# Kernel tuning notes

Measured on AMD Instinct MI355X. Metric: run time of the kernel, lower is better.

The kernel has to match this reference:

```python
import jax, jax.numpy as jnp
import numpy as np
from jax import lax

STRIDE = (1, 1)
PADDING = ((1, 1), (1, 1))


@jax.custom_vjp
def ternary_quantize(w):
    """Quantize OIHW weights to {-1,0,+1} with per-output-channel scale alpha."""
    abs_w = jnp.abs(w)
    delta = 0.7 * abs_w.mean(axis=(1, 2, 3), keepdims=True)          # [O,1,1,1]
    ternary = jnp.where(w > delta, 1.0, jnp.where(w < -delta, -1.0, 0.0)).astype(w.dtype)
    mask = ternary != 0
    count = jnp.maximum(mask.sum(axis=(1, 2, 3), keepdims=True), 1).astype(w.dtype)
    alpha = (abs_w * mask.astype(w.dtype)).sum(axis=(1, 2, 3), keepdims=True) / count
    return ternary, alpha


def _tq_fwd(w):
    return ternary_quantize(w), w


def _tq_bwd(w, grads):
    g_ternary, _g_alpha = grads  # STE: grad_alpha is discarded
    g = jnp.where(jnp.abs(w) > 1.0, 0.0, g_ternary)
    return (g,)


ternary_quantize.defvjp(_tq_fwd, _tq_bwd)


def setup_inputs() -> dict:
    key = jax.random.key(0)
    kx, kw = jax.random.split(key)
    x = jax.random.normal(kx, (32, 256, 56, 56), dtype=jnp.float32)
    # kaiming_normal fan_out: std = sqrt(2 / (out_ch * kH * kW))
    std = np.sqrt(2.0 / (256 * 3 * 3)).astype(np.float32)
    weight = jax.random.normal(kw, (256, 256, 3, 3), dtype=jnp.float32) * std
    return {"x": x, "weight": weight}


def reference(x, weight):
    ternary, alpha = ternary_quantize(weight)
    scaled_w = alpha * ternary  # values in {-alpha_o, 0, +alpha_o}
    return lax.conv_general_dilated(
        x, scaled_w,
        window_strides=STRIDE,
        padding=PADDING,
        dimension_numbers=("NCHW", "OIHW", "NCHW"),
    )
```

## Files before the change

### kernel.cpp

```cpp
#include <hip/hip_runtime.h>
#include <hip/hip_bf16.h>

typedef unsigned short u16;
typedef __bf16 bf16x8 __attribute__((ext_vector_type(8)));
typedef float f32x4 __attribute__((ext_vector_type(4)));
typedef u16 u16x8 __attribute__((ext_vector_type(8)));

__device__ __forceinline__ u16 f2bf(float f) {
    __bf16 h = (__bf16)f;
    return __builtin_bit_cast(unsigned short, h);
}

__device__ __forceinline__ void gl_lds16(const u16* g, u16* l) {
    __builtin_amdgcn_global_load_lds(
        (const __attribute__((address_space(1))) void*)g,
        (__attribute__((address_space(3))) void*)l, 16, 0, 0);
}

__global__ __launch_bounds__(256) void prep_kernel(
        const float* __restrict__ x, const float* __restrict__ w,
        u16* __restrict__ xp, u16* __restrict__ wp,
        float* __restrict__ alpha) {
    __shared__ double red[4];
    __shared__ double red2[4];
    __shared__ int    redc[4];

    int bid = blockIdx.x;
    int t = threadIdx.x;

    if (bid < 256) {
        int o = bid;
        const float* wo = w + (size_t)o * 2304;
        float v[9];
        double asum = 0.0;
        #pragma unroll
        for (int i = 0; i < 9; ++i) { v[i] = wo[t * 9 + i]; asum += fabs((double)v[i]); }
        #pragma unroll
        for (int off = 32; off > 0; off >>= 1) asum += __shfl_down(asum, off, 64);
        int wv = t >> 6, lane = t & 63;
        if (lane == 0) red[wv] = asum;
        __syncthreads();
        double delta = 0.7 * ((red[0] + red[1] + red[2] + red[3]) / 2304.0);

        int mt = o >> 7, ol = o & 127;
        int ks = (t >> 3) & 7, c = t & 7;
        double msum = 0.0; int cnt = 0;
        #pragma unroll
        for (int i = 0; i < 9; ++i) {
            double f = (double)v[i];
            float tv = 0.f;
            if (f > delta) tv = 1.f;
            else if (f < -delta) tv = -1.f;
            if (tv != 0.f) { msum += fabs(f); cnt++; }
            int kc = i * 4 + (t >> 6);
            wp[((((size_t)mt * 36 + kc) * 8 + ks) * 128 + ol) * 8 + c] = f2bf(tv);
        }
        #pragma unroll
        for (int off = 32; off > 0; off >>= 1) {
            msum += __shfl_down(msum, off, 64);
            cnt  += __shfl_down(cnt,  off, 64);
        }
        if (lane == 0) { red2[wv] = msum; redc[wv] = cnt; }
        __syncthreads();
        if (t == 0) {
            double ms = red2[0] + red2[1] + red2[2] + red2[3];
            int cn = redc[0] + redc[1] + redc[2] + redc[3];
            alpha[o] = (float)(ms / (double)(cn > 0 ? cn : 1));
        }
        return;
    }

    int pbid = bid - 256;
    int img  = pbid & 31;
    int cihi = (pbid >> 5) & 31;
    int z    = pbid >> 10;

    if (z == 12 && t >= 64) {
        int bt = t - 64;
        if (bt < 228) {
            int hp, wl;
            if (bt < 58)       { hp = 0;            wl = bt; }
            else if (bt < 116) { hp = 57;           wl = bt - 58; }
            else if (bt < 172) { hp = bt - 116 + 1; wl = 0; }
            else               { hp = bt - 172 + 1; wl = 57; }
            u16x8 zv = {};
            *(u16x8*)(xp + (((size_t)(img * 32 + cihi) * 58 + hp) * 58 + wl) * 8) = zv;
        }
        return;
    }

    int c = z * 256 + t;
    int h = c / 56, wq = c - h * 56;
    const float* xb = x + ((size_t)(img * 256 + cihi * 8)) * 3136 + c;
    u16x8 ov;
    #pragma unroll
    for (int j = 0; j < 8; ++j) ov[j] = f2bf(xb[(size_t)j * 3136]);
    *(u16x8*)(xp + (((size_t)(img * 32 + cihi) * 58 + (h + 1)) * 58 + (wq + 1)) * 8) = ov;
}

#define STAGE_CHUNK(KC, LA, LB) do {                                        \
    int f_ = (KC) >> 2;                                                      \
    int kh_ = f_ / 3, kw_ = f_ - kh_ * 3;                                    \
    int ci8_ = ((KC) & 3) * 8;                                               \
    unsigned bhw_ = (unsigned)kh_ * 464u + (unsigned)kw_ * 8u;               \
    unsigned bo0_ = (unsigned)(ci8_ + s0) * 26912u + bhw_;                   \
    unsigned bo1_ = (unsigned)(ci8_ + s1) * 26912u + bhw_;                   \
    const u16* aC_ = aTile + (size_t)(KC) * 8192;                            \
    _Pragma("unroll")                                                        \
    for (int q_ = 0; q_ < 4; ++q_) {                                         \
        int seg_ = wave * 4 + q_;                                            \
        gl_lds16(aC_ + seg_ * 512 + lane * 8, (LA) + seg_ * 512);            \
    }                                                                        \
    gl_lds16(bB0 + bo0_, (LB) + s0 * 1024);                                  \
    gl_lds16(bB1 + bo0_, (LB) + s0 * 1024 + 512);                            \
    gl_lds16(bB0 + bo1_, (LB) + s1 * 1024);                                  \
    gl_lds16(bB1 + bo1_, (LB) + s1 * 1024 + 512);                            \
} while (0)

#define HALF_ITER(LA, LB, VMSTR, STAGE_KC, DO_STAGE) do {                    \
    asm volatile("s_waitcnt " VMSTR ::: "memory");                           \
    __builtin_amdgcn_sched_barrier(0);                                       \
    __builtin_amdgcn_s_barrier();                                            \
    __builtin_amdgcn_sched_barrier(0);                                       \
    bf16x8 af_[2][4], bf_[2][4];                                             \
    _Pragma("unroll")                                                        \
    for (int kk_ = 0; kk_ < 2; ++kk_) {                                      \
        int ks_ = kk_ * 4 + quad;                                            \
        _Pragma("unroll")                                                    \
        for (int i_ = 0; i_ < 4; ++i_)                                       \
            af_[kk_][i_] = *(const bf16x8*)&(LA)[(ks_ * 128 + wm + i_ * 16 + row16) * 8]; \
        _Pragma("unroll")                                                    \
        for (int j_ = 0; j_ < 4; ++j_)                                       \
            bf_[kk_][j_] = *(const bf16x8*)&(LB)[(ks_ * 128 + wn + j_ * 16 + row16) * 8]; \
    }                                                                        \
    __builtin_amdgcn_sched_barrier(0);                                       \
    asm volatile("s_waitcnt lgkmcnt(0)" ::: "memory");                       \
    __builtin_amdgcn_sched_barrier(0);                                       \
    __builtin_amdgcn_s_barrier();                                            \
    __builtin_amdgcn_sched_barrier(0);                                       \
    if (DO_STAGE) STAGE_CHUNK(STAGE_KC, LA, LB);                             \
    __builtin_amdgcn_s_setprio(1);                                           \
    _Pragma("unroll")                                                        \
    for (int kk_ = 0; kk_ < 2; ++kk_)                                        \
        _Pragma("unroll")                                                    \
        for (int i_ = 0; i_ < 4; ++i_)                                       \
            _Pragma("unroll")                                                \
            for (int j_ = 0; j_ < 4; ++j_)                                   \
                acc[i_][j_] = __builtin_amdgcn_mfma_f32_16x16x32_bf16(       \
                                af_[kk_][i_], bf_[kk_][j_], acc[i_][j_], 0, 0, 0); \
    __builtin_amdgcn_s_setprio(0);                                           \
} while (0)

__global__ __launch_bounds__(256, 2) void conv_gemm(
        const u16* __restrict__ Wp, const u16* __restrict__ Xp,
        const float* __restrict__ alpha, float* __restrict__ out) {
    __shared__ u16 lsA0[8 * 128 * 8];
    __shared__ u16 lsA1[8 * 128 * 8];
    __shared__ u16 lsB0[8 * 128 * 8];
    __shared__ u16 lsB1[8 * 128 * 8];

    int bid = blockIdx.x;
    int xcd = bid & 7, idx = bid >> 3;
    int mt = idx & 1;
    unsigned nt = (unsigned)(xcd * 98 + (idx >> 1));
    int o_base = mt * 128;
    unsigned sp_base = nt * 128u;

    int t = threadIdx.x;
    int lane = t & 63, wave = t >> 6;
    int wm = (wave >> 1) * 64, wn = (wave & 1) * 64;

    const u16* aTile = Wp + (size_t)mt * 294912;

    unsigned sp0 = sp_base + (unsigned)lane;
    unsigned sp1 = sp0 + 64u;
    unsigned img0 = sp0 / 3136u, rem0 = sp0 - img0 * 3136u;
    unsigned oh0 = rem0 / 56u,   ow0 = rem0 - oh0 * 56u;
    unsigned img1 = sp1 / 3136u, rem1 = sp1 - img1 * 3136u;
    unsigned oh1 = rem1 / 56u,   ow1 = rem1 - oh1 * 56u;
    const u16* bB0 = Xp + ((size_t)(img0 * 32) * 58 + oh0) * 58 * 8 + ow0 * 8;
    const u16* bB1 = Xp + ((size_t)(img1 * 32) * 58 + oh1) * 58 * 8 + ow1 * 8;

    int s0 = wave * 2, s1 = s0 + 1;

    f32x4 acc[4][4] = {};
    int row16 = lane & 15, quad = lane >> 4;

    STAGE_CHUNK(0, lsA0, lsB0);
    STAGE_CHUNK(1, lsA1, lsB1);

    #pragma unroll 1
    for (int kc = 0; kc < 34; kc += 2) {
        HALF_ITER(lsA0, lsB0, "vmcnt(8)", kc + 2, true);
        HALF_ITER(lsA1, lsB1, "vmcnt(8)", kc + 3, true);
    }
    HALF_ITER(lsA0, lsB0, "vmcnt(8)", 0, false);
    HALF_ITER(lsA1, lsB1, "vmcnt(0)", 0, false);

    int col = lane & 15;
    float al[4][4];
    #pragma unroll
    for (int i = 0; i < 4; ++i)
        #pragma unroll
        for (int rg = 0; rg < 4; ++rg)
            al[i][rg] = alpha[o_base + wm + i * 16 + quad * 4 + rg];

    #pragma unroll
    for (int j = 0; j < 4; ++j) {
        unsigned sp = sp_base + (unsigned)(wn + j * 16 + col);
        unsigned img = sp / 3136u;
        unsigned spi = sp - img * 3136u;
        float* ob = out + (size_t)img * 256 * 3136 + spi;
        #pragma unroll
        for (int i = 0; i < 4; ++i) {
            int o = o_base + wm + i * 16 + quad * 4;
            #pragma unroll
            for (int rg = 0; rg < 4; ++rg)
                ob[(size_t)(o + rg) * 3136] = acc[i][j][rg] * al[i][rg];
        }
    }
}

extern "C" void kernel_launch(void* const* d_in, const int* in_sizes, int n_in,
                              void* d_out, int out_size, void* d_ws, size_t ws_size,
                              hipStream_t stream) {
    const float* x = (const float*)d_in[0];
    const float* w = (const float*)d_in[1];
    float* out = (float*)d_out;

    char* ws = (char*)d_ws;
    u16*   xp    = (u16*)ws;
    u16*   wp    = (u16*)(ws + 55115776);
    float* alpha = (float*)(ws + 55115776 + 1179648);

    prep_kernel<<<256 + 32 * 32 * 13, 256, 0, stream>>>(x, w, xp, wp, alpha);
    conv_gemm<<<784 * 2, 256, 0, stream>>>(wp, xp, alpha, out);
}
```

Measured before the change: 308.8 us.

## Load weight fragments directly from global memory, drop A LDS staging, raise occupancy

Weight (A) tiles are no longer staged through LDS. Each wave now reads its A fragments straight from global memory (the pre-packed layout), which halves shared memory use. Launch bounds rise from 2 to 4 blocks per CU. The B tile is still double-buffered in LDS, but the wait now drains all outstanding loads (vmcnt(0)) before each stage. Global A reads are on the critical path right before the MFMAs, so latency could be exposed despite the extra occupancy and register pressure is tighter.

```diff
diff --git a/kernel.cpp b/kernel.cpp
--- a/kernel.cpp
+++ b/kernel.cpp
@@ -98,47 +98,44 @@
     *(u16x8*)(xp + (((size_t)(img * 32 + cihi) * 58 + (h + 1)) * 58 + (wq + 1)) * 8) = ov;
 }
 
-#define STAGE_CHUNK(KC, LA, LB) do {                                        \
+#define SB __builtin_amdgcn_sched_barrier(0)
+
+#define STAGE_B(KC, LB) do {                                                 \
     int f_ = (KC) >> 2;                                                      \
     int kh_ = f_ / 3, kw_ = f_ - kh_ * 3;                                    \
     int ci8_ = ((KC) & 3) * 8;                                               \
     unsigned bhw_ = (unsigned)kh_ * 464u + (unsigned)kw_ * 8u;               \
     unsigned bo0_ = (unsigned)(ci8_ + s0) * 26912u + bhw_;                   \
     unsigned bo1_ = (unsigned)(ci8_ + s1) * 26912u + bhw_;                   \
-    const u16* aC_ = aTile + (size_t)(KC) * 8192;                            \
-    _Pragma("unroll")                                                        \
-    for (int q_ = 0; q_ < 4; ++q_) {                                         \
-        int seg_ = wave * 4 + q_;                                            \
-        gl_lds16(aC_ + seg_ * 512 + lane * 8, (LA) + seg_ * 512);            \
-    }                                                                        \
     gl_lds16(bB0 + bo0_, (LB) + s0 * 1024);                                  \
     gl_lds16(bB1 + bo0_, (LB) + s0 * 1024 + 512);                            \
     gl_lds16(bB0 + bo1_, (LB) + s1 * 1024);                                  \
     gl_lds16(bB1 + bo1_, (LB) + s1 * 1024 + 512);                            \
 } while (0)
 
-#define HALF_ITER(LA, LB, VMSTR, STAGE_KC, DO_STAGE) do {                    \
-    asm volatile("s_waitcnt " VMSTR ::: "memory");                           \
-    __builtin_amdgcn_sched_barrier(0);                                       \
+#define CONV_BODY(LB, AKC, SKC, DO_STAGE) do {                               \
     __builtin_amdgcn_s_barrier();                                            \
-    __builtin_amdgcn_sched_barrier(0);                                       \
+    SB;                                                                      \
     bf16x8 af_[2][4], bf_[2][4];                                             \
+    const u16* aC_ = aTile + (size_t)(AKC) * 8192;                           \
     _Pragma("unroll")                                                        \
     for (int kk_ = 0; kk_ < 2; ++kk_) {                                      \
         int ks_ = kk_ * 4 + quad;                                            \
         _Pragma("unroll")                                                    \
         for (int i_ = 0; i_ < 4; ++i_)                                       \
-            af_[kk_][i_] = *(const bf16x8*)&(LA)[(ks_ * 128 + wm + i_ * 16 + row16) * 8]; \
+            af_[kk_][i_] = *(const bf16x8*)&aC_[(ks_ * 128 + wm + i_ * 16 + row16) * 8]; \
         _Pragma("unroll")                                                    \
         for (int j_ = 0; j_ < 4; ++j_)                                       \
             bf_[kk_][j_] = *(const bf16x8*)&(LB)[(ks_ * 128 + wn + j_ * 16 + row16) * 8]; \
     }                                                                        \
-    __builtin_amdgcn_sched_barrier(0);                                       \
+    SB;                                                                      \
     asm volatile("s_waitcnt lgkmcnt(0)" ::: "memory");                       \
-    __builtin_amdgcn_sched_barrier(0);                                       \
+    SB;                                                                      \
     __builtin_amdgcn_s_barrier();                                            \
-    __builtin_amdgcn_sched_barrier(0);                                       \
-    if (DO_STAGE) STAGE_CHUNK(STAGE_KC, LA, LB);                             \
+    SB;                                                                      \
+    asm volatile("s_waitcnt vmcnt(0)" ::: "memory");                         \
+    SB;                                                                      \
+    if (DO_STAGE) STAGE_B(SKC, LB);                                          \
     __builtin_amdgcn_s_setprio(1);                                           \
     _Pragma("unroll")                                                        \
     for (int kk_ = 0; kk_ < 2; ++kk_)                                        \
@@ -151,11 +148,9 @@
     __builtin_amdgcn_s_setprio(0);                                           \
 } while (0)
 
-__global__ __launch_bounds__(256, 2) void conv_gemm(
+__global__ __launch_bounds__(256, 4) void conv_gemm(
         const u16* __restrict__ Wp, const u16* __restrict__ Xp,
         const float* __restrict__ alpha, float* __restrict__ out) {
-    __shared__ u16 lsA0[8 * 128 * 8];
-    __shared__ u16 lsA1[8 * 128 * 8];
     __shared__ u16 lsB0[8 * 128 * 8];
     __shared__ u16 lsB1[8 * 128 * 8];
 
@@ -186,16 +181,19 @@
     f32x4 acc[4][4] = {};
     int row16 = lane & 15, quad = lane >> 4;
 
-    STAGE_CHUNK(0, lsA0, lsB0);
-    STAGE_CHUNK(1, lsA1, lsB1);
+    STAGE_B(0, lsB0);
+    STAGE_B(1, lsB1);
+    SB;
+    asm volatile("s_waitcnt vmcnt(4)" ::: "memory");
+    SB;
 
     #pragma unroll 1
     for (int kc = 0; kc < 34; kc += 2) {
-        HALF_ITER(lsA0, lsB0, "vmcnt(8)", kc + 2, true);
-        HALF_ITER(lsA1, lsB1, "vmcnt(8)", kc + 3, true);
-    }
-    HALF_ITER(lsA0, lsB0, "vmcnt(8)", 0, false);
-    HALF_ITER(lsA1, lsB1, "vmcnt(0)", 0, false);
+        CONV_BODY(lsB0, kc,     kc + 2, true);
+        CONV_BODY(lsB1, kc + 1, kc + 3, true);
+    }
+    CONV_BODY(lsB0, 34, 0, false);
+    CONV_BODY(lsB1, 35, 0, false);
 
     int col = lane & 15;
     float al[4][4];
```

Result: slower. 676.8 us (+119.2%).
